# Optimization experiments

Measured on AMD Instinct MI355X. Metric: run time of the kernel, lower is better.

The kernel has to match this reference:

```python
import jax, jax.numpy as jnp
import numpy as np

# Shapes / hyperparams (match init_kwargs and input_specs)
B, CIN, COUT, H, W = 8, 128, 128, 64, 64
K, S, P, D = 3, 1, 1, 1
KK = K * K
EPS = 1e-5  # BatchNorm eps


def setup_inputs() -> dict:
    key = jax.random.key(0)
    ks = jax.random.split(key, 4)
    x = jax.random.normal(ks[0], (B, CIN, H, W), jnp.float32)
    # small offset weights so predicted offsets stay O(1) pixels
    w_off = jax.random.normal(ks[1], (2 * KK, CIN, K, K), jnp.float32) * 0.01
    w_def = jax.random.normal(ks[2], (COUT, CIN, K, K), jnp.float32) * (1.0 / np.sqrt(CIN * KK))
    b_def = jax.random.normal(ks[3], (COUT,), jnp.float32) * 0.01
    gamma = jnp.ones((COUT,), jnp.float32)
    beta = jnp.zeros((COUT,), jnp.float32)
    return dict(x=x, w_off=w_off, w_def=w_def, b_def=b_def, gamma=gamma, beta=beta)


def _bilinear_gather(x, ys, xs):
    """x: [B,C,H,W]; ys/xs: [B,KK,Ho,Wo] float coords -> [B,C,KK,Ho,Wo].
    Zero padding outside the image (torchvision DeformConv2d semantics)."""
    Bb, C, Hh, Ww = x.shape
    y0 = jnp.floor(ys)
    x0 = jnp.floor(xs)
    wy = ys - y0
    wx = xs - x0
    xf = x.reshape(Bb, C, Hh * Ww)

    def gather(yi, xi, w):
        valid = (yi >= 0) & (yi < Hh) & (xi >= 0) & (xi < Ww)
        idx = (jnp.clip(yi, 0, Hh - 1) * Ww + jnp.clip(xi, 0, Ww - 1)).astype(jnp.int32)
        g = jnp.take_along_axis(xf, idx.reshape(Bb, 1, -1), axis=2)  # [B,C,KK*Ho*Wo]
        g = g.reshape(Bb, C, *idx.shape[1:])  # [B,C,KK,Ho,Wo]
        return g * (w * valid)[:, None]

    return (gather(y0, x0, (1 - wy) * (1 - wx))
            + gather(y0, x0 + 1, (1 - wy) * wx)
            + gather(y0 + 1, x0, wy * (1 - wx))
            + gather(y0 + 1, x0 + 1, wy * wx))


def _forward(x, w_off, w_def, b_def, gamma, beta):
    # 1) offset prediction: standard conv, no bias
    offset = jax.lax.conv_general_dilated(
        x, w_off, window_strides=(S, S), padding=((P, P), (P, P)),
        rhs_dilation=(D, D), dimension_numbers=('NCHW', 'OIHW', 'NCHW'))
    Ho, Wo = offset.shape[2], offset.shape[3]
    off = offset.reshape(B, KK, 2, Ho, Wo)  # (dy, dx) pairs per kernel loc
    dy, dx = off[:, :, 0], off[:, :, 1]

    # 2) deformable sampling coordinates
    ky = (jnp.arange(KK) // K).astype(jnp.float32) * D  # kernel row offset
    kx = (jnp.arange(KK) % K).astype(jnp.float32) * D   # kernel col offset
    base_y = (jnp.arange(Ho) * S - P).astype(jnp.float32)
    base_x = (jnp.arange(Wo) * S - P).astype(jnp.float32)
    ys = base_y[None, None, :, None] + ky[None, :, None, None] + dy  # [B,KK,Ho,Wo]
    xs = base_x[None, None, None, :] + kx[None, :, None, None] + dx

    sampled = _bilinear_gather(x, ys, xs)  # [B,CIN,KK,Ho,Wo]

    # 3) per-kernel-location weighted accumulation (implicit GEMM) + bias
    out = jnp.einsum('bckhw,ock->bohw', sampled, w_def.reshape(COUT, CIN, KK))
    out = out + b_def[None, :, None, None]

    # 4) BatchNorm2d (training mode: batch statistics) + SiLU
    mean = out.mean(axis=(0, 2, 3))
    var = out.var(axis=(0, 2, 3))
    scale = gamma / jnp.sqrt(var + EPS)
    out = (out - mean[None, :, None, None]) * scale[None, :, None, None] + beta[None, :, None, None]
    return out * jax.nn.sigmoid(out)  # SiLU


def reference(x, w_off, w_def, b_def, gamma, beta):
    return _forward(x, w_off, w_def, b_def, gamma, beta)
```

## Files before the change

### kernel.cpp

```cpp
#include <hip/hip_runtime.h>
#include <math.h>

#define CIN   128
#define COUT  128
#define KKT   9
#define NSTAT 32768.0f

typedef __attribute__((ext_vector_type(8))) short bf16x8;
typedef __attribute__((ext_vector_type(4))) float f32x4;

__device__ inline unsigned short f2bf(float f) {
    union { float f; unsigned u; } v; v.f = f;
    unsigned r = v.u + 0x7fffu + ((v.u >> 16) & 1u);
    return (unsigned short)(r >> 16);
}
__device__ inline float bflo(unsigned u) { union { unsigned u; float f; } v; v.u = u << 16; return v.f; }
__device__ inline float bfhi(unsigned u) { union { unsigned u; float f; } v; v.u = u & 0xffff0000u; return v.f; }

#define FAST_BARRIER() asm volatile("s_waitcnt lgkmcnt(0)\n\ts_barrier" ::: "memory")


__global__ __launch_bounds__(512) void prep_xt_k(const float* __restrict__ x,
                                                 unsigned* __restrict__ xt) {
    __shared__ float lt[128][65];
    const int by = blockIdx.x;
    const int b = by >> 6, y = by & 63;
    const int t = threadIdx.x, l = t & 63, g8 = t >> 6;
    const float* xb = x + (b * 128) * 4096 + y * 64;
#pragma unroll
    for (int pass = 0; pass < 16; pass++) {
        int c = pass * 8 + g8;
        lt[c][l] = xb[c * 4096 + l];
    }
    __syncthreads();
    unsigned* xo = xt + (by * 64) * 64;
#pragma unroll
    for (int pass = 0; pass < 8; pass++) {
        int w = pass * 8 + g8;
        float f0 = lt[2 * l][w], f1 = lt[2 * l + 1][w];
        xo[w * 64 + l] = (unsigned)f2bf(f0) | ((unsigned)f2bf(f1) << 16);
    }
}

__global__ __launch_bounds__(256) void repack_w_k(const float* __restrict__ w_def,
                                                  const float* __restrict__ w_off,
                                                  unsigned short* __restrict__ wb,
                                                  unsigned short* __restrict__ wob,
                                                  float* __restrict__ sums) {
    int i = blockIdx.x * 256 + threadIdx.x;
    if (i < 147456) {
        int oc = i / 1152, r = i - oc * 1152, kt = r >> 7, c = r & 127;
        wb[i] = f2bf(w_def[(oc * 128 + c) * 9 + kt]);
    } else if (i < 147456 + 36864) {
        int j = i - 147456;
        int ocp = j / 1152, r = j - ocp * 1152, kt = r >> 7, c = r & 127;
        wob[j] = (ocp < 18) ? f2bf(w_off[(ocp * 128 + c) * 9 + kt]) : (unsigned short)0;
    } else if (i < 147456 + 36864 + 256) {
        sums[i - 147456 - 36864] = 0.f;
    }
}

#define RB 51200
__global__ __launch_bounds__(512, 4) void deform_main_k(const unsigned* __restrict__ xt,
                                                        const unsigned short* __restrict__ wb,
                                                        const unsigned short* __restrict__ wob,
                                                        const float* __restrict__ b_def,
                                                        float* __restrict__ out,
                                                        float* __restrict__ sums,
                                                        float* __restrict__ sumsq) {
    __shared__ __align__(16) unsigned char smem[RB + 4608 + 1024];
    unsigned short* xrow = (unsigned short*)smem;
    int*            tab  = (int*)smem;
    unsigned short* samp0 = (unsigned short*)(smem + 18432);
    unsigned short* samp1 = (unsigned short*)(smem + 34816);
    float* offl = (float*)(smem + RB);
    float* stat = (float*)(smem + RB + 4608);

    const int t    = threadIdx.x;
    const int bh   = blockIdx.x;
    const int b    = bh >> 6;
    const int j_   = bh & 63;
    const int h    = ((j_ & 7) << 3) | (j_ >> 3);
    const int lane = t & 63;
    const int wv   = __builtin_amdgcn_readfirstlane(t >> 6);
    const int quad = lane >> 4, lo = lane & 15;
    const int l    = lane;
    const int g    = lane >> 2;

    if (t < 256) stat[t] = 0.f;

    const unsigned* xtb = xt + b * 262144;

    for (int p = wv; p < 198; p += 8) {
        int r = p / 66, xi = p - r * 66;
        int y = h + r - 1, x = xi - 1;
        unsigned u = 0;
        if ((unsigned)y < 64u && (unsigned)x < 64u) u = xtb[(y * 64 + x) * 64 + l];
        ((unsigned*)xrow)[(r * 66 + xi) * 64 + ((g ^ (xi & 15)) << 2) + (l & 3)] = u;
    }
    __syncthreads();

    {
        const int mt = wv >> 2, nt = wv & 3;
        f32x4 ao = {0.f, 0.f, 0.f, 0.f};
        const unsigned short* wrow = wob + (mt * 16 + lo) * 1152 + quad * 8;
        for (int kt = 0; kt < 9; kt++) {
            int ky = kt / 3, kx = kt - ky * 3;
            int xi = nt * 16 + lo + kx;
#pragma unroll
            for (int ch = 0; ch < 4; ch++) {
                int gg = ch * 4 + quad;
                bf16x8 af = *(const bf16x8*)(wrow + kt * 128 + ch * 32);
                bf16x8 bf = *(const bf16x8*)(xrow + (ky * 66 + xi) * 128 + ((gg ^ (xi & 15)) << 3));
                ao = __builtin_amdgcn_mfma_f32_16x16x32_bf16(af, bf, ao, 0, 0, 0);
            }
        }
        __syncthreads();
#pragma unroll
        for (int r = 0; r < 4; r++) {
            int oc = mt * 16 + quad * 4 + r;
            if (oc < 18) offl[oc * 64 + nt * 16 + lo] = ao[r];
        }
    }
    __syncthreads();

    for (int i = t; i < KKT * 64; i += 512) {
        int k = i >> 6, w2 = i & 63;
        float dy = offl[(2 * k) * 64 + w2];
        float dx = offl[(2 * k + 1) * 64 + w2];
        int ky = k / 3, kx = k - ky * 3;
        float ys = (float)(h - 1 + ky) + dy;
        float xs = (float)(w2 - 1 + kx) + dx;
        float y0f = floorf(ys), x0f = floorf(xs);
        float wyf = ys - y0f, wxf = xs - x0f;
        int iy0 = (int)y0f, ix0 = (int)x0f;
        int cy0 = min(max(iy0, 0), 63), cy1 = min(max(iy0 + 1, 0), 63);
        int px  = min(max(ix0, 0), 63), px2 = min(max(ix0 + 1, 0), 63);
        float wy0 = (iy0 >= 0 && iy0 < 64) ? (1.f - wyf) : 0.f;
        float wy1 = (iy0 + 1 >= 0 && iy0 + 1 < 64) ? wyf : 0.f;
        float wa  = (ix0 >= 0 && ix0 < 64) ? (1.f - wxf) : 0.f;
        float wbv = (ix0 + 1 >= 0 && ix0 + 1 < 64) ? wxf : 0.f;
        int base = i * 8;
        tab[base + 0] = (cy0 * 64 + px ) * 64;
        tab[base + 1] = (cy0 * 64 + px2) * 64;
        tab[base + 2] = (cy1 * 64 + px ) * 64;
        tab[base + 3] = (cy1 * 64 + px2) * 64;
        ((float*)tab)[base + 4] = wy0;
        ((float*)tab)[base + 5] = wy1;
        ((float*)tab)[base + 6] = wa;
        ((float*)tab)[base + 7] = wbv;
    }
    __syncthreads();

    const int m0 = wv >> 1, n0 = wv & 1;
    f32x4 acc[2][2];
#pragma unroll
    for (int i = 0; i < 2; i++)
#pragma unroll
        for (int j = 0; j < 2; j++)
#pragma unroll
            for (int r = 0; r < 4; r++) acc[i][j][r] = 0.f;

    const unsigned short* wrow0 = wb + (2 * m0 * 16 + lo) * 1152 + quad * 8;
    const unsigned short* wrow1 = wrow0 + 16 * 1152;

    for (int kt = 0; kt < KKT; kt++) {
        bf16x8 af0[4], af1[4];
#pragma unroll
        for (int ch = 0; ch < 4; ch++) {
            af0[ch] = *(const bf16x8*)(wrow0 + kt * 128 + ch * 32);
            af1[ch] = *(const bf16x8*)(wrow1 + kt * 128 + ch * 32);
        }
        unsigned* sb = (unsigned*)((kt & 1) ? samp1 : samp0);
#pragma unroll
        for (int i = 0; i < 8; i++) {
            int w = wv * 8 + i;
            int bse = (kt * 64 + w) * 8;
            int4   ta = *(const int4*)&tab[bse];
            float4 tw = *(const float4*)&tab[bse + 4];
            unsigned u00 = xtb[ta.x + l];
            unsigned u01 = xtb[ta.y + l];
            unsigned u10 = xtb[ta.z + l];
            unsigned u11 = xtb[ta.w + l];
            float e = tw.x * (tw.z * bflo(u00) + tw.w * bflo(u01)) +
                      tw.y * (tw.z * bflo(u10) + tw.w * bflo(u11));
            float o = tw.x * (tw.z * bfhi(u00) + tw.w * bfhi(u01)) +
                      tw.y * (tw.z * bfhi(u10) + tw.w * bfhi(u11));
            sb[w * 64 + ((g ^ (w & 15)) << 2) + (l & 3)] =
                (unsigned)f2bf(e) | ((unsigned)f2bf(o) << 16);
        }
        FAST_BARRIER();
        const unsigned short* sbs = (kt & 1) ? samp1 : samp0;
#pragma unroll
        for (int ch = 0; ch < 4; ch++) {
            int gg = ch * 4 + quad;
            int r0 = (2 * n0 + 0) * 16 + lo, r1 = (2 * n0 + 1) * 16 + lo;
            bf16x8 bf0 = *(const bf16x8*)(sbs + r0 * 128 + ((gg ^ lo) << 3));
            bf16x8 bf1 = *(const bf16x8*)(sbs + r1 * 128 + ((gg ^ lo) << 3));
            acc[0][0] = __builtin_amdgcn_mfma_f32_16x16x32_bf16(af0[ch], bf0, acc[0][0], 0, 0, 0);
            acc[0][1] = __builtin_amdgcn_mfma_f32_16x16x32_bf16(af0[ch], bf1, acc[0][1], 0, 0, 0);
            acc[1][0] = __builtin_amdgcn_mfma_f32_16x16x32_bf16(af1[ch], bf0, acc[1][0], 0, 0, 0);
            acc[1][1] = __builtin_amdgcn_mfma_f32_16x16x32_bf16(af1[ch], bf1, acc[1][1], 0, 0, 0);
        }
    }

    float* ob = out + b * COUT * 4096 + h * 64;
#pragma unroll
    for (int mt2 = 0; mt2 < 2; mt2++) {
        int ocb = (2 * m0 + mt2) * 16 + quad * 4;
#pragma unroll
        for (int r = 0; r < 4; r++) {
            int oc = ocb + r;
            float bia = b_def[oc];
            float ssum = 0.f, qsum = 0.f;
#pragma unroll
            for (int nt2 = 0; nt2 < 2; nt2++) {
                int w_ = (2 * n0 + nt2) * 16 + lo;
                float v = acc[mt2][nt2][r] + bia;
                ob[oc * 4096 + w_] = v;
                ssum += v; qsum += v * v;
            }
#pragma unroll
            for (int d = 1; d < 16; d <<= 1) {
                ssum += __shfl_xor(ssum, d, 64);
                qsum += __shfl_xor(qsum, d, 64);
            }
            if (lo == 0) { atomicAdd(&stat[oc], ssum); atomicAdd(&stat[128 + oc], qsum); }
        }
    }
    __syncthreads();
    if (t < 256) {
        float* gp = (t < 128) ? (sums + t) : (sumsq + (t - 128));
        atomicAdd(gp, stat[t]);
    }
}

__global__ __launch_bounds__(256) void bn_silu_k(float* __restrict__ out,
                                                 const float* __restrict__ sums,
                                                 const float* __restrict__ sumsq,
                                                 const float* __restrict__ gamma,
                                                 const float* __restrict__ beta) {
    __shared__ float sc_s[128], sh_s[128];
    int t = threadIdx.x;
    if (t < 128) {
        const float invN = 1.f / NSTAT;
        float m = sums[t] * invN;
        float v = fmaf(-m, m, sumsq[t] * invN);
        float sc = gamma[t] * rsqrtf(v + 1e-5f);
        sc_s[t] = sc;
        sh_s[t] = beta[t] - m * sc;
    }
    __syncthreads();
    int i = blockIdx.x * 256 + t;
    float4 v = ((float4*)out)[i];
    int oc = (i >> 10) & 127;
    float sc = sc_s[oc], sh = sh_s[oc];
    float z0 = v.x * sc + sh;
    float z1 = v.y * sc + sh;
    float z2 = v.z * sc + sh;
    float z3 = v.w * sc + sh;
    v.x = z0 / (1.f + __expf(-z0));
    v.y = z1 / (1.f + __expf(-z1));
    v.z = z2 / (1.f + __expf(-z2));
    v.w = z3 / (1.f + __expf(-z3));
    ((float4*)out)[i] = v;
}

extern "C" void kernel_launch(void* const* d_in, const int* in_sizes, int n_in,
                              void* d_out, int out_size, void* d_ws, size_t ws_size,
                              hipStream_t stream) {
    const float* x     = (const float*)d_in[0];
    const float* w_off = (const float*)d_in[1];
    const float* w_def = (const float*)d_in[2];
    const float* b_def = (const float*)d_in[3];
    const float* gamma = (const float*)d_in[4];
    const float* beta  = (const float*)d_in[5];
    float* out = (float*)d_out;

    unsigned*       xt   = (unsigned*)d_ws;
    unsigned short* wb   = (unsigned short*)((char*)d_ws + 16777216);
    unsigned short* wob  = (unsigned short*)((char*)d_ws + 17072128);
    float*          sums = (float*)((char*)d_ws + 17145856);
    float*          sumsq = sums + 128;

    prep_xt_k<<<512, 512, 0, stream>>>(x, xt);
    repack_w_k<<<721, 256, 0, stream>>>(w_def, w_off, wb, wob, sums);
    deform_main_k<<<512, 512, 0, stream>>>(xt, wb, wob, b_def, out, sums, sumsq);
    bn_silu_k<<<4096, 256, 0, stream>>>(out, sums, sumsq, gamma, beta);
}
```

Measured before the change: 167.9 us.

## Split deform conv blocks into half-row tiles and merge prep kernels

The main deformable conv kernel now gives each block half an output row (32 pixels) instead of a full row. That doubles the grid to 1024 blocks, shrinks LDS per block, and raises the occupancy hint from 4 to 8 blocks per CU. Only half the waves compute the offset conv, and each wave does half as many MFMA tiles. The x-transpose and weight-repack kernels are fused into one launch to remove a kernel launch. The trade-off is that each block still loads the full weight set and adds a halo, so global weight traffic per output and relative halo overhead both go up.

New measurement: 187.3 us. +11.5%, slower.

```diff
diff --git a/kernel.cpp b/kernel.cpp
--- a/kernel.cpp
+++ b/kernel.cpp
@@ -20,67 +20,71 @@
 #define FAST_BARRIER() asm volatile("s_waitcnt lgkmcnt(0)\n\ts_barrier" ::: "memory")
 
 
-__global__ __launch_bounds__(512) void prep_xt_k(const float* __restrict__ x,
-                                                 unsigned* __restrict__ xt) {
-    __shared__ float lt[128][65];
-    const int by = blockIdx.x;
-    const int b = by >> 6, y = by & 63;
-    const int t = threadIdx.x, l = t & 63, g8 = t >> 6;
-    const float* xb = x + (b * 128) * 4096 + y * 64;
-#pragma unroll
-    for (int pass = 0; pass < 16; pass++) {
-        int c = pass * 8 + g8;
-        lt[c][l] = xb[c * 4096 + l];
-    }
-    __syncthreads();
-    unsigned* xo = xt + (by * 64) * 64;
-#pragma unroll
-    for (int pass = 0; pass < 8; pass++) {
-        int w = pass * 8 + g8;
-        float f0 = lt[2 * l][w], f1 = lt[2 * l + 1][w];
-        xo[w * 64 + l] = (unsigned)f2bf(f0) | ((unsigned)f2bf(f1) << 16);
-    }
-}
-
-__global__ __launch_bounds__(256) void repack_w_k(const float* __restrict__ w_def,
+__global__ __launch_bounds__(512) void prep_all_k(const float* __restrict__ x,
+                                                  const float* __restrict__ w_def,
                                                   const float* __restrict__ w_off,
+                                                  unsigned* __restrict__ xt,
                                                   unsigned short* __restrict__ wb,
                                                   unsigned short* __restrict__ wob,
                                                   float* __restrict__ sums) {
-    int i = blockIdx.x * 256 + threadIdx.x;
-    if (i < 147456) {
-        int oc = i / 1152, r = i - oc * 1152, kt = r >> 7, c = r & 127;
-        wb[i] = f2bf(w_def[(oc * 128 + c) * 9 + kt]);
-    } else if (i < 147456 + 36864) {
-        int j = i - 147456;
-        int ocp = j / 1152, r = j - ocp * 1152, kt = r >> 7, c = r & 127;
-        wob[j] = (ocp < 18) ? f2bf(w_off[(ocp * 128 + c) * 9 + kt]) : (unsigned short)0;
-    } else if (i < 147456 + 36864 + 256) {
-        sums[i - 147456 - 36864] = 0.f;
-    }
-}
-
-#define RB 51200
-__global__ __launch_bounds__(512, 4) void deform_main_k(const unsigned* __restrict__ xt,
+    const int blk = blockIdx.x;
+    if (blk < 512) {
+        __shared__ float lt[128][65];
+        const int by = blk;
+        const int b = by >> 6, y = by & 63;
+        const int t = threadIdx.x, l = t & 63, g8 = t >> 6;
+        const float* xb = x + (b * 128) * 4096 + y * 64;
+#pragma unroll
+        for (int pass = 0; pass < 16; pass++) {
+            int c = pass * 8 + g8;
+            lt[c][l] = xb[c * 4096 + l];
+        }
+        __syncthreads();
+        unsigned* xo = xt + (by * 64) * 64;
+#pragma unroll
+        for (int pass = 0; pass < 8; pass++) {
+            int w = pass * 8 + g8;
+            float f0 = lt[2 * l][w], f1 = lt[2 * l + 1][w];
+            xo[w * 64 + l] = (unsigned)f2bf(f0) | ((unsigned)f2bf(f1) << 16);
+        }
+    } else {
+        int i = (blk - 512) * 512 + threadIdx.x;
+        if (i < 147456) {
+            int oc = i / 1152, r = i - oc * 1152, kt = r >> 7, c = r & 127;
+            wb[i] = f2bf(w_def[(oc * 128 + c) * 9 + kt]);
+        } else if (i < 147456 + 36864) {
+            int j = i - 147456;
+            int ocp = j / 1152, r = j - ocp * 1152, kt = r >> 7, c = r & 127;
+            wob[j] = (ocp < 18) ? f2bf(w_off[(ocp * 128 + c) * 9 + kt]) : (unsigned short)0;
+        } else if (i < 147456 + 36864 + 256) {
+            sums[i - 147456 - 36864] = 0.f;
+        }
+    }
+}
+
+__global__ __launch_bounds__(512, 8) void deform_main_k(const unsigned* __restrict__ xt,
                                                         const unsigned short* __restrict__ wb,
                                                         const unsigned short* __restrict__ wob,
                                                         const float* __restrict__ b_def,
                                                         float* __restrict__ out,
                                                         float* __restrict__ sums,
                                                         float* __restrict__ sumsq) {
-    __shared__ __align__(16) unsigned char smem[RB + 4608 + 1024];
-    unsigned short* xrow = (unsigned short*)smem;
-    int*            tab  = (int*)smem;
-    unsigned short* samp0 = (unsigned short*)(smem + 18432);
-    unsigned short* samp1 = (unsigned short*)(smem + 34816);
-    float* offl = (float*)(smem + RB);
-    float* stat = (float*)(smem + RB + 4608);
+    __shared__ __align__(16) unsigned char smem[29440];
+    unsigned short* xrow  = (unsigned short*)smem;
+    int*            tab   = (int*)smem;
+    unsigned short* samp0 = (unsigned short*)(smem + 9216);
+    unsigned short* samp1 = (unsigned short*)(smem + 17408);
+    float* offl = (float*)(smem + 26112);
+    float* stat = (float*)(smem + 28416);
 
     const int t    = threadIdx.x;
     const int bh   = blockIdx.x;
-    const int b    = bh >> 6;
-    const int j_   = bh & 63;
+    const int b    = bh >> 7;
+    const int r7   = bh & 127;
+    const int j_   = r7 >> 1;
+    const int half = r7 & 1;
     const int h    = ((j_ & 7) << 3) | (j_ >> 3);
+    const int w0   = half * 32;
     const int lane = t & 63;
     const int wv   = __builtin_amdgcn_readfirstlane(t >> 6);
     const int quad = lane >> 4, lo = lane & 15;
@@ -91,27 +95,28 @@
 
     const unsigned* xtb = xt + b * 262144;
 
-    for (int p = wv; p < 198; p += 8) {
-        int r = p / 66, xi = p - r * 66;
-        int y = h + r - 1, x = xi - 1;
+    for (int p = wv; p < 102; p += 8) {
+        int r = p / 34, xi = p - r * 34;
+        int y = h + r - 1, xp = w0 - 1 + xi;
         unsigned u = 0;
-        if ((unsigned)y < 64u && (unsigned)x < 64u) u = xtb[(y * 64 + x) * 64 + l];
-        ((unsigned*)xrow)[(r * 66 + xi) * 64 + ((g ^ (xi & 15)) << 2) + (l & 3)] = u;
-    }
-    __syncthreads();
-
-    {
-        const int mt = wv >> 2, nt = wv & 3;
+        if ((unsigned)y < 64u && (unsigned)xp < 64u) u = xtb[(y * 64 + xp) * 64 + l];
+        ((unsigned*)xrow)[(r * 34 + xi) * 64 + ((g ^ (xi & 15)) << 2) + (l & 3)] = u;
+    }
+    __syncthreads();
+
+    if (wv < 4) {
+        const int mt = wv >> 1, nt = wv & 1;
+        const int wl = nt * 16 + lo;
         f32x4 ao = {0.f, 0.f, 0.f, 0.f};
         const unsigned short* wrow = wob + (mt * 16 + lo) * 1152 + quad * 8;
         for (int kt = 0; kt < 9; kt++) {
             int ky = kt / 3, kx = kt - ky * 3;
-            int xi = nt * 16 + lo + kx;
+            int xi = wl + kx;
 #pragma unroll
             for (int ch = 0; ch < 4; ch++) {
                 int gg = ch * 4 + quad;
                 bf16x8 af = *(const bf16x8*)(wrow + kt * 128 + ch * 32);
-                bf16x8 bf = *(const bf16x8*)(xrow + (ky * 66 + xi) * 128 + ((gg ^ (xi & 15)) << 3));
+                bf16x8 bf = *(const bf16x8*)(xrow + (ky * 34 + xi) * 128 + ((gg ^ (xi & 15)) << 3));
                 ao = __builtin_amdgcn_mfma_f32_16x16x32_bf16(af, bf, ao, 0, 0, 0);
             }
         }
@@ -119,18 +124,21 @@
 #pragma unroll
         for (int r = 0; r < 4; r++) {
             int oc = mt * 16 + quad * 4 + r;
-            if (oc < 18) offl[oc * 64 + nt * 16 + lo] = ao[r];
-        }
-    }
-    __syncthreads();
-
-    for (int i = t; i < KKT * 64; i += 512) {
-        int k = i >> 6, w2 = i & 63;
-        float dy = offl[(2 * k) * 64 + w2];
-        float dx = offl[(2 * k + 1) * 64 + w2];
+            if (oc < 18) offl[oc * 32 + wl] = ao[r];
+        }
+    } else {
+        __syncthreads();
+    }
+    __syncthreads();
+
+    for (int i = t; i < KKT * 32; i += 512) {
+        int k = i >> 5, w2l = i & 31;
+        int w2g = w0 + w2l;
+        float dy = offl[(2 * k) * 32 + w2l];
+        float dx = offl[(2 * k + 1) * 32 + w2l];
         int ky = k / 3, kx = k - ky * 3;
         float ys = (float)(h - 1 + ky) + dy;
-        float xs = (float)(w2 - 1 + kx) + dx;
+        float xs = (float)(w2g - 1 + kx) + dx;
         float y0f = floorf(ys), x0f = floorf(xs);
         float wyf = ys - y0f, wxf = xs - x0f;
         int iy0 = (int)y0f, ix0 = (int)x0f;
@@ -153,13 +161,11 @@
     __syncthreads();
 
     const int m0 = wv >> 1, n0 = wv & 1;
-    f32x4 acc[2][2];
+    f32x4 acc[2];
 #pragma unroll
     for (int i = 0; i < 2; i++)
 #pragma unroll
-        for (int j = 0; j < 2; j++)
-#pragma unroll
-            for (int r = 0; r < 4; r++) acc[i][j][r] = 0.f;
+        for (int r = 0; r < 4; r++) acc[i][r] = 0.f;
 
     const unsigned short* wrow0 = wb + (2 * m0 * 16 + lo) * 1152 + quad * 8;
     const unsigned short* wrow1 = wrow0 + 16 * 1152;
@@ -173,9 +179,9 @@
         }
         unsigned* sb = (unsigned*)((kt & 1) ? samp1 : samp0);
 #pragma unroll
-        for (int i = 0; i < 8; i++) {
-            int w = wv * 8 + i;
-            int bse = (kt * 64 + w) * 8;
+        for (int i = 0; i < 4; i++) {
+            int wl = wv * 4 + i;
+            int bse = (kt * 32 + wl) * 8;
             int4   ta = *(const int4*)&tab[bse];
             float4 tw = *(const float4*)&tab[bse + 4];
             unsigned u00 = xtb[ta.x + l];
@@ -186,7 +192,7 @@
                       tw.y * (tw.z * bflo(u10) + tw.w * bflo(u11));
             float o = tw.x * (tw.z * bfhi(u00) + tw.w * bfhi(u01)) +
                       tw.y * (tw.z * bfhi(u10) + tw.w * bfhi(u11));
-            sb[w * 64 + ((g ^ (w & 15)) << 2) + (l & 3)] =
+            sb[wl * 64 + ((g ^ (wl & 15)) << 2) + (l & 3)] =
                 (unsigned)f2bf(e) | ((unsigned)f2bf(o) << 16);
         }
         FAST_BARRIER();
@@ -194,32 +200,24 @@
 #pragma unroll
         for (int ch = 0; ch < 4; ch++) {
             int gg = ch * 4 + quad;
-            int r0 = (2 * n0 + 0) * 16 + lo, r1 = (2 * n0 + 1) * 16 + lo;
+            int r0 = n0 * 16 + lo;
             bf16x8 bf0 = *(const bf16x8*)(sbs + r0 * 128 + ((gg ^ lo) << 3));
-            bf16x8 bf1 = *(const bf16x8*)(sbs + r1 * 128 + ((gg ^ lo) << 3));
-            acc[0][0] = __builtin_amdgcn_mfma_f32_16x16x32_bf16(af0[ch], bf0, acc[0][0], 0, 0, 0);
-            acc[0][1] = __builtin_amdgcn_mfma_f32_16x16x32_bf16(af0[ch], bf1, acc[0][1], 0, 0, 0);
-            acc[1][0] = __builtin_amdgcn_mfma_f32_16x16x32_bf16(af1[ch], bf0, acc[1][0], 0, 0, 0);
-            acc[1][1] = __builtin_amdgcn_mfma_f32_16x16x32_bf16(af1[ch], bf1, acc[1][1], 0, 0, 0);
+            acc[0] = __builtin_amdgcn_mfma_f32_16x16x32_bf16(af0[ch], bf0, acc[0], 0, 0, 0);
+            acc[1] = __builtin_amdgcn_mfma_f32_16x16x32_bf16(af1[ch], bf0, acc[1], 0, 0, 0);
         }
     }
 
     float* ob = out + b * COUT * 4096 + h * 64;
+    const int w_ = w0 + n0 * 16 + lo;
 #pragma unroll
     for (int mt2 = 0; mt2 < 2; mt2++) {
         int ocb = (2 * m0 + mt2) * 16 + quad * 4;
 #pragma unroll
         for (int r = 0; r < 4; r++) {
             int oc = ocb + r;
-            float bia = b_def[oc];
-            float ssum = 0.f, qsum = 0.f;
-#pragma unroll
-            for (int nt2 = 0; nt2 < 2; nt2++) {
-                int w_ = (2 * n0 + nt2) * 16 + lo;
-                float v = acc[mt2][nt2][r] + bia;
-                ob[oc * 4096 + w_] = v;
-                ssum += v; qsum += v * v;
-            }
+            float v = acc[mt2][r] + b_def[oc];
+            ob[oc * 4096 + w_] = v;
+            float ssum = v, qsum = v * v;
 #pragma unroll
             for (int d = 1; d < 16; d <<= 1) {
                 ssum += __shfl_xor(ssum, d, 64);
@@ -283,8 +281,7 @@
     float*          sums = (float*)((char*)d_ws + 17145856);
     float*          sumsq = sums + 128;
 
-    prep_xt_k<<<512, 512, 0, stream>>>(x, xt);
-    repack_w_k<<<721, 256, 0, stream>>>(w_def, w_off, wb, wob, sums);
-    deform_main_k<<<512, 512, 0, stream>>>(xt, wb, wob, b_def, out, sums, sumsq);
+    prep_all_k<<<873, 512, 0, stream>>>(x, w_def, w_off, xt, wb, wob, sums);
+    deform_main_k<<<1024, 512, 0, stream>>>(xt, wb, wob, b_def, out, sums, sumsq);
     bn_silu_k<<<4096, 256, 0, stream>>>(out, sums, sumsq, gamma, beta);
 }
```
